# Kernel optimization log

Hardware: AMD Instinct MI355X
Metric: run time of the kernel (lower is better)

The kernel has to match this reference:

```python
import jax, jax.numpy as jnp
import numpy as np

N, E, F, H, D, C = 50000, 800000, 128, 8, 16, 40


def setup_inputs() -> dict:
    key = jax.random.key(0)
    ks = jax.random.split(key, 12)
    s_in = 1.0 / np.sqrt(F)
    s_h = 1.0 / np.sqrt(H * D)
    return {
        "x": jax.random.normal(ks[0], (N, F), jnp.float32),
        "edge_index": jax.random.randint(ks[1], (2, E), 0, N, jnp.int64),
        "W1": jax.random.normal(ks[2], (F, H * D), jnp.float32) * s_in,
        "a_src1": jax.random.normal(ks[3], (H, D), jnp.float32) * s_h,
        "a_dst1": jax.random.normal(ks[4], (H, D), jnp.float32) * s_h,
        "b1": jnp.zeros((H * D,), jnp.float32),
        "W2": jax.random.normal(ks[5], (H * D, H * D), jnp.float32) * s_h,
        "a_src2": jax.random.normal(ks[6], (H, D), jnp.float32) * s_h,
        "a_dst2": jax.random.normal(ks[7], (H, D), jnp.float32) * s_h,
        "b2": jnp.zeros((H * D,), jnp.float32),
        "Wc": jax.random.normal(ks[8], (H * D, C), jnp.float32) * s_h,
        "bc": jnp.zeros((C,), jnp.float32),
    }


def _gat_layer(x, src, dst, W, a_src, a_dst, b):
    # x: [N, F_in]; src/dst: [E'] (self-loops already appended)
    n = x.shape[0]
    h, d = a_src.shape
    hx = (x @ W).reshape(n, h, d)                      # [N, H, D]
    al_src = jnp.einsum("nhd,hd->nh", hx, a_src)       # [N, H]
    al_dst = jnp.einsum("nhd,hd->nh", hx, a_dst)       # [N, H]
    e = jax.nn.leaky_relu(al_src[src] + al_dst[dst], 0.2)  # [E', H]
    # segment softmax over incoming edges of each destination node
    m = jax.ops.segment_max(e, dst, num_segments=n)    # [N, H]
    e = jnp.exp(e - m[dst])
    z = jax.ops.segment_sum(e, dst, num_segments=n)    # [N, H]
    alpha = e / z[dst]                                 # [E', H]
    out = jax.ops.segment_sum(alpha[:, :, None] * hx[src], dst, num_segments=n)
    return out.reshape(n, h * d) + b


def reference(x, edge_index, W1, a_src1, a_dst1, b1, W2, a_src2, a_dst2, b2, Wc, bc):
    n = x.shape[0]
    loops = jnp.arange(n, dtype=edge_index.dtype)
    src = jnp.concatenate([edge_index[0], loops])  # PyG GATConv adds self-loops
    dst = jnp.concatenate([edge_index[1], loops])
    h = _gat_layer(x, src, dst, W1, a_src1, a_dst1, b1)
    h = jax.nn.elu(h)  # ELU between layers (i < K-1); dropout=None -> no-op
    h = _gat_layer(h, src, dst, W2, a_src2, a_dst2, b2)
    return h @ Wc + bc  # [N, C] logits
```

## Files before the change

kernel.cpp:

```cpp
#include <hip/hip_runtime.h>
#include <hip/hip_bf16.h>
#include <hip/hip_fp16.h>


#define FDIM 128
#define HEADS 8

typedef short bf16x8 __attribute__((ext_vector_type(8)));
typedef float f32x4 __attribute__((ext_vector_type(4)));

typedef __attribute__((address_space(1))) const unsigned gu32;
typedef __attribute__((address_space(3))) unsigned lu32;

__device__ __forceinline__ void load_lds16(const void* g, void* l) {
    __builtin_amdgcn_global_load_lds((gu32*)g, (lu32*)l, 16, 0, 0);
}

__device__ __forceinline__ float leaky02(float x) {
    return fmaxf(x, 0.2f * x);
}

__device__ __forceinline__ unsigned pack2h(float x, float y) {
    __half2 h2 = __floats2half2_rn(x, y);
    return *(unsigned*)&h2;
}

__device__ __forceinline__ void split2(float x, unsigned short& hi, unsigned short& lo) {
    unsigned bits = __float_as_uint(x);
    unsigned h = bits + 0x7fffu + ((bits >> 16) & 1u);
    hi = (unsigned short)(h >> 16);
    float hf = __uint_as_float(h & 0xffff0000u);
    float r = x - hf;
    unsigned rb = __float_as_uint(r);
    unsigned l2 = rb + 0x7fffu + ((rb >> 16) & 1u);
    lo = (unsigned short)(l2 >> 16);
}


__global__ __launch_bounds__(256) void wconv_kernel(const float* __restrict__ W1,
                                                    const float* __restrict__ W2,
                                                    unsigned short* __restrict__ w1_hi,
                                                    unsigned short* __restrict__ w1_lo,
                                                    unsigned short* __restrict__ w2_hi,
                                                    unsigned short* __restrict__ w2_lo) {
    int b = blockIdx.x, t = threadIdx.x;
    const float* W = (b < 16) ? W1 : W2;
    unsigned short* whi = (b < 16) ? w1_hi : w2_hi;
    unsigned short* wlo = (b < 16) ? w1_lo : w2_lo;
    int idx = (b & 15) * 256 + t;
    int k = idx >> 5;
    int c0 = (idx & 31) * 4;
#pragma unroll
    for (int i = 0; i < 4; ++i) {
        int c = c0 + i;
        float v = W[k * FDIM + c];
        unsigned short h, l;
        split2(v, h, l);
        int dest = ((k >> 5) * 8 + (c >> 4)) * 512 +
                   ((c & 15) + (((k >> 3) & 3) << 4)) * 8 + (k & 7);
        whi[dest] = h;
        wlo[dest] = l;
    }
}


__global__ __launch_bounds__(256) void scan_partial(const int* __restrict__ deg,
                                                    int* __restrict__ partials,
                                                    int n) {
    __shared__ int red[256];
    int t = threadIdx.x;
    int base = blockIdx.x * 1024 + t * 4;
    int s = 0;
#pragma unroll
    for (int j = 0; j < 4; ++j) {
        int i = base + j;
        if (i < n) s += deg[i];
    }
    red[t] = s;
    __syncthreads();
    for (int off = 128; off > 0; off >>= 1) {
        if (t < off) red[t] += red[t + off];
        __syncthreads();
    }
    if (t == 0) partials[blockIdx.x] = red[0];
}

__global__ __launch_bounds__(256) void scan_final(const int* __restrict__ deg,
                                                  const int* __restrict__ partials,
                                                  int* __restrict__ row_start,
                                                  int n, int nb) {
    __shared__ int sbuf[256];
    __shared__ int boff_s, total_s;
    int t = threadIdx.x;
    if (t < 64) {
        int carry = 0;
        for (int base = 0; base < nb; base += 64) {
            int idx = base + t;
            int v = (idx < nb) ? partials[idx] : 0;
            int incl = v;
#pragma unroll
            for (int off = 1; off < 64; off <<= 1) {
                int x = __shfl_up(incl, off);
                if (t >= off) incl += x;
            }
            if (idx == (int)blockIdx.x) boff_s = carry + incl - v;
            carry += __shfl(incl, 63);
        }
        if (t == 0) total_s = carry;
    }
    __syncthreads();
    if (blockIdx.x == 0 && t == 0) row_start[n] = total_s;

    int base = blockIdx.x * 1024 + t * 4;
    int v[4];
#pragma unroll
    for (int j = 0; j < 4; ++j) v[j] = (base + j < n) ? deg[base + j] : 0;
    int tsum = v[0] + v[1] + v[2] + v[3];
    sbuf[t] = tsum;
    __syncthreads();
    for (int off = 1; off < 256; off <<= 1) {
        int tmp = (t >= off) ? sbuf[t - off] : 0;
        __syncthreads();
        sbuf[t] += tmp;
        __syncthreads();
    }
    int toff = boff_s + sbuf[t] - tsum;
    int run = 0;
#pragma unroll
    for (int j = 0; j < 4; ++j) {
        int i = base + j;
        if (i < n) row_start[i] = toff + run;
        run += v[j];
    }
}


__global__ __launch_bounds__(256) void scatter_kernel(const int* __restrict__ ei,
                                                      const int* __restrict__ rank,
                                                      const int* __restrict__ row_start,
                                                      int* __restrict__ csr_src,
                                                      int E) {
    int tid = threadIdx.x;
#pragma unroll
    for (int j = 0; j < 4; ++j) {
        int e = blockIdx.x * 1024 + j * 256 + tid;
        if (e < E) {
            int s = ei[e];
            int d = ei[E + e];
            __builtin_nontemporal_store(s, &csr_src[row_start[d] + rank[e]]);
        }
    }
}


template <bool FUSED>
__global__ __launch_bounds__(256, 3) void gemm_mfma(const float* __restrict__ xf,
                                                    const unsigned short* __restrict__ a_hi,
                                                    const unsigned short* __restrict__ a_lo,
                                                    const unsigned short* __restrict__ w_hi,
                                                    const unsigned short* __restrict__ w_lo,
                                                    const float* __restrict__ asrc,
                                                    const float* __restrict__ adst,
                                                    float* __restrict__ als,
                                                    float* __restrict__ ald,
                                                    unsigned* __restrict__ hxf,
                                                    int n,
                                                    const int* __restrict__ ei,
                                                    int* __restrict__ deg,
                                                    int* __restrict__ rank,
                                                    int E, int ng, int grid) {
    __shared__ __align__(16) char smem[49152];
    int tid = threadIdx.x;
    int gb;
    if (FUSED) {
        int bid = blockIdx.x;
        int t0 = (int)((long long)bid * ng / grid);
        int t1 = (int)((long long)(bid + 1) * ng / grid);
        if (t1 == t0) {
            int sb = bid - t0;
#pragma unroll
            for (int j = 0; j < 4; ++j) {
                int e = sb * 1024 + j * 256 + tid;
                if (e < E) rank[e] = atomicAdd(&deg[ei[E + e]], 1);
            }
            return;
        }
        gb = t0;
    } else {
        gb = blockIdx.x;
    }

    int lane = tid & 63;
    int wave = tid >> 6;
    int l15 = lane & 15;
    int lg = lane >> 4;
    int row0 = gb * 32;

    {
#pragma unroll
        for (int c = 0; c < 4; ++c) {
            int s = wave * 4 + c;
            int kc = s >> 2, fr = (s >> 1) & 1, p = s & 1;
            int rg = row0 + fr * 16 + l15;
            if (rg > n - 1) rg = n - 1;
            if (FUSED) {
                load_lds16(xf + (size_t)rg * FDIM + kc * 32 + lg * 8 + p * 4,
                           smem + (size_t)s * 1024);
            } else {
                const unsigned short* src = p ? a_lo : a_hi;
                load_lds16(src + (size_t)rg * FDIM + kc * 32 + lg * 8,
                           smem + (size_t)s * 1024);
            }
        }
    }

    auto stage_B = [&](int kc, int buf) {
#pragma unroll
        for (int c = 0; c < 4; ++c) {
            int s = wave * 4 + c;
            int FC = s >> 1, p = s & 1;
            const unsigned short* src = p ? w_lo : w_hi;
            load_lds16(src + (size_t)(kc * 8 + FC) * 512 + lane * 8,
                       smem + 16384 + (size_t)buf * 16384 + (size_t)(FC * 2 + p) * 1024);
        }
    };
    stage_B(0, 0);
    __syncthreads();

    f32x4 acc[2][2];
#pragma unroll
    for (int fr = 0; fr < 2; ++fr)
#pragma unroll
        for (int fc = 0; fc < 2; ++fc)
#pragma unroll
            for (int r = 0; r < 4; ++r) acc[fr][fc][r] = 0.f;

#pragma unroll
    for (int kc = 0; kc < 4; ++kc) {
        const int cur = kc & 1;
        if (kc < 3) stage_B(kc + 1, cur ^ 1);

        bf16x8 Ah[2], Al[2];
#pragma unroll
        for (int fr = 0; fr < 2; ++fr) {
            if (FUSED) {
                const float4 v0 = *(const float4*)(smem + (size_t)(kc * 4 + fr * 2) * 1024 + lane * 16);
                const float4 v1 = *(const float4*)(smem + (size_t)(kc * 4 + fr * 2 + 1) * 1024 + lane * 16);
                float vv[8] = {v0.x, v0.y, v0.z, v0.w, v1.x, v1.y, v1.z, v1.w};
#pragma unroll
                for (int j = 0; j < 8; ++j) {
                    unsigned bits = __float_as_uint(vv[j]);
                    Ah[fr][j] = (short)(bits >> 16);
                    float hf = __uint_as_float(bits & 0xffff0000u);
                    Al[fr][j] = (short)(__float_as_uint(vv[j] - hf) >> 16);
                }
            } else {
                Ah[fr] = *(const bf16x8*)(smem + (size_t)(kc * 4 + fr * 2) * 1024 + lane * 16);
                Al[fr] = *(const bf16x8*)(smem + (size_t)(kc * 4 + fr * 2 + 1) * 1024 + lane * 16);
            }
        }
        bf16x8 Bh[2], Bl[2];
#pragma unroll
        for (int fc = 0; fc < 2; ++fc) {
            int FC = wave * 2 + fc;
            const char* bb = smem + 16384 + (size_t)cur * 16384 + (size_t)(FC * 2) * 1024;
            Bh[fc] = *(const bf16x8*)(bb + lane * 16);
            Bl[fc] = *(const bf16x8*)(bb + 1024 + lane * 16);
        }
#pragma unroll
        for (int fr = 0; fr < 2; ++fr)
#pragma unroll
            for (int fc = 0; fc < 2; ++fc) {
                acc[fr][fc] = __builtin_amdgcn_mfma_f32_16x16x32_bf16(
                    Al[fr], Bh[fc], acc[fr][fc], 0, 0, 0);
                acc[fr][fc] = __builtin_amdgcn_mfma_f32_16x16x32_bf16(
                    Ah[fr], Bl[fc], acc[fr][fc], 0, 0, 0);
                acc[fr][fc] = __builtin_amdgcn_mfma_f32_16x16x32_bf16(
                    Ah[fr], Bh[fc], acc[fr][fc], 0, 0, 0);
            }
        __syncthreads();
    }

    float* dump = (float*)(smem + 16384);
#pragma unroll
    for (int fr = 0; fr < 2; ++fr)
#pragma unroll
        for (int fc = 0; fc < 2; ++fc) {
            int col = wave * 32 + fc * 16 + l15;
#pragma unroll
            for (int reg = 0; reg < 4; ++reg) {
                int row = fr * 16 + lg * 4 + reg;
                dump[row * 132 + col] = acc[fr][fc][reg];
            }
        }
    __syncthreads();

    {
        int row = tid >> 3;
        int hd = tid & 7;
        int row_g = row0 + row;
        const float* src = dump + row * 132 + hd * 16;
        float v[16];
#pragma unroll
        for (int j = 0; j < 4; ++j)
            *(float4*)&v[j * 4] = *(const float4*)(src + j * 4);

        if (row_g < n) {
            uint4 p0, p1;
            p0.x = pack2h(v[0], v[1]);
            p0.y = pack2h(v[2], v[3]);
            p0.z = pack2h(v[4], v[5]);
            p0.w = pack2h(v[6], v[7]);
            p1.x = pack2h(v[8], v[9]);
            p1.y = pack2h(v[10], v[11]);
            p1.z = pack2h(v[12], v[13]);
            p1.w = pack2h(v[14], v[15]);
            unsigned* dst = hxf + (size_t)row_g * 64 + hd * 8;
            *(uint4*)dst = p0;
            *(uint4*)(dst + 4) = p1;

            float s0 = 0.f, s1 = 0.f;
#pragma unroll
            for (int j = 0; j < 16; ++j) {
                s0 += v[j] * asrc[hd * 16 + j];
                s1 += v[j] * adst[hd * 16 + j];
            }
            als[row_g * HEADS + hd] = s0;
            ald[row_g * HEADS + hd] = s1;
        }
    }
}


__global__ __launch_bounds__(256, 8) void gemm_cls(const unsigned* __restrict__ h_f16,
                                                   const float* __restrict__ W,
                                                   const float* __restrict__ bias,
                                                   float* __restrict__ out,
                                                   int n) {
    __shared__ float xs[32][136];
    __shared__ float ws[32][48];
    int tid = threadIdx.x;
    int row0 = blockIdx.x * 128;
    int lane = tid & 63;
    int wave = tid >> 6;
    int lane2 = lane * 2;
    int wc = wave * 10;

    float acc[2][10];
#pragma unroll
    for (int i = 0; i < 2; ++i)
#pragma unroll
        for (int j = 0; j < 10; ++j) acc[i][j] = 0.f;

    for (int kc = 0; kc < 128; kc += 32) {
        if (kc) __syncthreads();
#pragma unroll
        for (int it = 0; it < 4; ++it) {
            int idx = it * 256 + tid;
            int r = idx >> 3, kg = (idx & 7) * 4;
            float4 v = make_float4(0.f, 0.f, 0.f, 0.f);
            if (row0 + r < n) {
                uint2 hh = *(const uint2*)&h_f16[(size_t)(row0 + r) * 64 + (kc + kg) / 2];
                float2 a = __half22float2(*(__half2*)&hh.x);
                float2 b = __half22float2(*(__half2*)&hh.y);
                v.x = a.x; v.y = a.y; v.z = b.x; v.w = b.y;
            }
            int col = r ^ kg;
            xs[kg + 0][col] = v.x;
            xs[kg + 1][col] = v.y;
            xs[kg + 2][col] = v.z;
            xs[kg + 3][col] = v.w;
        }
#pragma unroll
        for (int it = 0; it < 6; ++it) {
            int idx = it * 256 + tid;
            int kk = idx / 48, c = idx - kk * 48;
            ws[kk][c] = (c < 40) ? W[(size_t)(kc + kk) * 40 + c] : 0.f;
        }
        __syncthreads();
#pragma unroll
        for (int k = 0; k < 32; ++k) {
            int s = ((k >> 2) & 7) << 2;
            float2 av2 = *(const float2*)&xs[k][lane2 ^ s];
            float av[2] = {av2.x, av2.y};
#pragma unroll
            for (int j = 0; j < 10; ++j) {
                float w = ws[k][wc + j];
                acc[0][j] += av[0] * w;
                acc[1][j] += av[1] * w;
            }
        }
    }

#pragma unroll
    for (int i = 0; i < 2; ++i) {
        int row = row0 + lane2 + i;
        if (row < n) {
#pragma unroll
            for (int j = 0; j < 10; ++j)
                out[(size_t)row * 40 + wc + j] = acc[i][j] + bias[wc + j];
        }
    }
}


template <bool DOELU, bool WRITELO>
__global__ __launch_bounds__(256) void gat_aggregate(const unsigned* __restrict__ hxf,
                                                     const float* __restrict__ als,
                                                     const float* __restrict__ ald,
                                                     const int* __restrict__ row_start,
                                                     const int* __restrict__ csr_src,
                                                     const float* __restrict__ bias,
                                                     unsigned* __restrict__ h_hi,
                                                     unsigned* __restrict__ h_lo,
                                                     int n) {
    int wid = threadIdx.x >> 6;
    int lane = threadIdx.x & 63;
    int node = blockIdx.x * 4 + wid;
    if (node >= n) return;

    int rs = row_start[node];
    int deg = row_start[node + 1] - rs;

    int h = lane & 7;
    int hc = lane >> 3;
    int lq = lane >> 3;
    float ald_h = ald[node * HEADS + h];

    float acc0 = 0.f, acc1 = 0.f, zown = 0.f;
    int total = deg + 1;

    int ii = lq;
    int srcv = (ii < deg) ? csr_src[rs + ii] : node;
    float w = (ii < total) ? __expf(leaky02(als[srcv * HEADS + h] + ald_h)) : 0.f;

    int i0 = 0;
    for (; i0 + 8 <= total; i0 += 8) {
        zown += w;
        int ii_n = i0 + 8 + lq;
        int srcv_n = (ii_n < deg) ? csr_src[rs + ii_n] : node;
#pragma unroll
        for (int e = 0; e < 8; ++e) {
            int s = __builtin_amdgcn_readlane(srcv, e * 8);
            float we = __shfl(w, e * 8 + hc);
            unsigned v = hxf[(size_t)s * 64 + lane];
            float2 f = __half22float2(*(__half2*)&v);
            acc0 += we * f.x;
            acc1 += we * f.y;
        }
        float w_n = (ii_n < total) ? __expf(leaky02(als[srcv_n * HEADS + h] + ald_h)) : 0.f;
        srcv = srcv_n;
        w = w_n;
    }
    int rem = total - i0;
    if (rem > 0) {
        zown += w;
        for (int e = 0; e < rem; ++e) {
            int s = __builtin_amdgcn_readlane(srcv, e * 8);
            float we = __shfl(w, e * 8 + hc);
            unsigned v = hxf[(size_t)s * 64 + lane];
            float2 f = __half22float2(*(__half2*)&v);
            acc0 += we * f.x;
            acc1 += we * f.y;
        }
    }

    zown += __shfl_xor(zown, 8);
    zown += __shfl_xor(zown, 16);
    zown += __shfl_xor(zown, 32);
    float z = __shfl(zown, hc);

    float2 bv = *(const float2*)&bias[2 * lane];
    float o0 = acc0 / z + bv.x;
    float o1 = acc1 / z + bv.y;
    if (DOELU) {
        o0 = o0 > 0.f ? o0 : (__expf(o0) - 1.f);
        o1 = o1 > 0.f ? o1 : (__expf(o1) - 1.f);
    }
    if (WRITELO) {
        unsigned short hh0, ll0, hh1, ll1;
        split2(o0, hh0, ll0);
        split2(o1, hh1, ll1);
        h_hi[(size_t)node * 64 + lane] = (unsigned)hh0 | ((unsigned)hh1 << 16);
        h_lo[(size_t)node * 64 + lane] = (unsigned)ll0 | ((unsigned)ll1 << 16);
    } else {
        h_hi[(size_t)node * 64 + lane] = pack2h(o0, o1);
    }
}


extern "C" void kernel_launch(void* const* d_in, const int* in_sizes, int n_in,
                              void* d_out, int out_size, void* d_ws, size_t ws_size,
                              hipStream_t stream) {
    const float* x      = (const float*)d_in[0];
    const int*   ei     = (const int*)d_in[1];
    const float* W1     = (const float*)d_in[2];
    const float* a_src1 = (const float*)d_in[3];
    const float* a_dst1 = (const float*)d_in[4];
    const float* b1     = (const float*)d_in[5];
    const float* W2     = (const float*)d_in[6];
    const float* a_src2 = (const float*)d_in[7];
    const float* a_dst2 = (const float*)d_in[8];
    const float* b2     = (const float*)d_in[9];
    const float* Wc     = (const float*)d_in[10];
    const float* bc     = (const float*)d_in[11];
    float* out = (float*)d_out;

    const int N = in_sizes[0] / FDIM;
    const int E = in_sizes[1] / 2;
    const int NB = (N + 1023) / 1024;

    unsigned* hxf = (unsigned*)d_ws;
    unsigned* xh_u = hxf + (size_t)N * 64;
    unsigned* xl_u = xh_u + (size_t)N * 64;
    float* als  = (float*)(xl_u + (size_t)N * 64);
    float* ald  = als + (size_t)N * HEADS;
    unsigned short* w1_hi = (unsigned short*)(ald + (size_t)N * HEADS);
    unsigned short* w1_lo = w1_hi + 16384;
    unsigned short* w2_hi = w1_lo + 16384;
    unsigned short* w2_lo = w2_hi + 16384;
    int* deg       = (int*)(w2_lo + 16384);
    int* row_start = deg + N;
    int* partials  = row_start + ((N + 8) & ~3);
    int* rank      = partials + ((NB + 4) & ~3);
    int* csr_src   = rank + E;

    hipMemsetAsync(deg, 0, (size_t)N * sizeof(int), stream);
    wconv_kernel<<<32, 256, 0, stream>>>(W1, W2, w1_hi, w1_lo, w2_hi, w2_lo);

    const int ng = (N + 31) / 32;
    const int hb = (E + 1023) / 1024;
    const int grid1 = ng + hb;
    const int agg_grid = (N + 3) / 4;
    const int cls_grid = (N + 127) / 128;

    gemm_mfma<true><<<grid1, 256, 0, stream>>>(x, nullptr, nullptr,
                                               w1_hi, w1_lo,
                                               a_src1, a_dst1, als, ald, hxf, N,
                                               ei, deg, rank, E, ng, grid1);
    scan_partial<<<NB, 256, 0, stream>>>(deg, partials, N);
    scan_final<<<NB, 256, 0, stream>>>(deg, partials, row_start, N, NB);
    scatter_kernel<<<hb, 256, 0, stream>>>(ei, rank, row_start, csr_src, E);

    gat_aggregate<true, true><<<agg_grid, 256, 0, stream>>>(
        hxf, als, ald, row_start, csr_src, b1, xh_u, xl_u, N);
    gemm_mfma<false><<<ng, 256, 0, stream>>>(nullptr,
                                             (const unsigned short*)xh_u,
                                             (const unsigned short*)xl_u,
                                             w2_hi, w2_lo,
                                             a_src2, a_dst2, als, ald, hxf, N,
                                             nullptr, nullptr, nullptr, 0, ng, ng);
    gat_aggregate<false, false><<<agg_grid, 256, 0, stream>>>(
        hxf, als, ald, row_start, csr_src, b2, xh_u, xl_u, N);
    gemm_cls<<<cls_grid, 256, 0, stream>>>(xh_u, Wc, bc, out, N);
}
```

Measured before the change: 207.4 us.

## Split layer-1 GEMM to overlap CSR scatter and merge scan kernels

The first-layer projection GEMM is now split into two halves. The degree-counting rider blocks run alongside the first half, and the CSR scatter rider blocks run alongside the second half, which removes the standalone scatter launch. The two-pass scan is merged into one kernel in which each block recomputes its prefix offset by summing every earlier degree entry. That redundant prefix sum costs O(N) reads per block, which grows with block index, in exchange for one fewer launch and no partials buffer.

```diff
diff --git a/kernel.cpp b/kernel.cpp
--- a/kernel.cpp
+++ b/kernel.cpp
@@ -64,54 +64,30 @@
 }
 
 
-__global__ __launch_bounds__(256) void scan_partial(const int* __restrict__ deg,
-                                                    int* __restrict__ partials,
-                                                    int n) {
+__global__ __launch_bounds__(256) void scan_fused(const int* __restrict__ deg,
+                                                  int* __restrict__ row_start,
+                                                  int n, int nb) {
     __shared__ int red[256];
+    __shared__ int sbuf[256];
+    __shared__ int boff_s;
     int t = threadIdx.x;
-    int base = blockIdx.x * 1024 + t * 4;
+    int b = blockIdx.x;
+
+    int limit = b * 1024;
+    if (limit > n) limit = n;
     int s = 0;
-#pragma unroll
-    for (int j = 0; j < 4; ++j) {
-        int i = base + j;
-        if (i < n) s += deg[i];
-    }
+    for (int i = t; i < limit; i += 256) s += deg[i];
     red[t] = s;
     __syncthreads();
     for (int off = 128; off > 0; off >>= 1) {
         if (t < off) red[t] += red[t + off];
         __syncthreads();
     }
-    if (t == 0) partials[blockIdx.x] = red[0];
-}
-
-__global__ __launch_bounds__(256) void scan_final(const int* __restrict__ deg,
-                                                  const int* __restrict__ partials,
-                                                  int* __restrict__ row_start,
-                                                  int n, int nb) {
-    __shared__ int sbuf[256];
-    __shared__ int boff_s, total_s;
-    int t = threadIdx.x;
-    if (t < 64) {
-        int carry = 0;
-        for (int base = 0; base < nb; base += 64) {
-            int idx = base + t;
-            int v = (idx < nb) ? partials[idx] : 0;
-            int incl = v;
-#pragma unroll
-            for (int off = 1; off < 64; off <<= 1) {
-                int x = __shfl_up(incl, off);
-                if (t >= off) incl += x;
-            }
-            if (idx == (int)blockIdx.x) boff_s = carry + incl - v;
-            carry += __shfl(incl, 63);
-        }
-        if (t == 0) total_s = carry;
-    }
+    if (t == 0) boff_s = red[0];
     __syncthreads();
-    if (blockIdx.x == 0 && t == 0) row_start[n] = total_s;
-
-    int base = blockIdx.x * 1024 + t * 4;
+    int boff = boff_s;
+
+    int base = b * 1024 + t * 4;
     int v[4];
 #pragma unroll
     for (int j = 0; j < 4; ++j) v[j] = (base + j < n) ? deg[base + j] : 0;
@@ -124,7 +100,7 @@
         sbuf[t] += tmp;
         __syncthreads();
     }
-    int toff = boff_s + sbuf[t] - tsum;
+    int toff = boff + sbuf[t] - tsum;
     int run = 0;
 #pragma unroll
     for (int j = 0; j < 4; ++j) {
@@ -132,28 +108,11 @@
         if (i < n) row_start[i] = toff + run;
         run += v[j];
     }
-}
-
-
-__global__ __launch_bounds__(256) void scatter_kernel(const int* __restrict__ ei,
-                                                      const int* __restrict__ rank,
-                                                      const int* __restrict__ row_start,
-                                                      int* __restrict__ csr_src,
-                                                      int E) {
-    int tid = threadIdx.x;
-#pragma unroll
-    for (int j = 0; j < 4; ++j) {
-        int e = blockIdx.x * 1024 + j * 256 + tid;
-        if (e < E) {
-            int s = ei[e];
-            int d = ei[E + e];
-            __builtin_nontemporal_store(s, &csr_src[row_start[d] + rank[e]]);
-        }
-    }
-}
-
-
-template <bool FUSED>
+    if (b == nb - 1 && t == 255) row_start[n] = boff + sbuf[255];
+}
+
+
+template <bool FUSED, int RIDER>
 __global__ __launch_bounds__(256, 3) void gemm_mfma(const float* __restrict__ xf,
                                                     const unsigned short* __restrict__ a_hi,
                                                     const unsigned short* __restrict__ a_lo,
@@ -168,26 +127,37 @@
                                                     const int* __restrict__ ei,
                                                     int* __restrict__ deg,
                                                     int* __restrict__ rank,
-                                                    int E, int ng, int grid) {
+                                                    const int* __restrict__ row_start,
+                                                    int* __restrict__ csr_src,
+                                                    int E, int ntiles, int tbase,
+                                                    int grid) {
     __shared__ __align__(16) char smem[49152];
     int tid = threadIdx.x;
     int gb;
-    if (FUSED) {
+    if (RIDER != 0) {
         int bid = blockIdx.x;
-        int t0 = (int)((long long)bid * ng / grid);
-        int t1 = (int)((long long)(bid + 1) * ng / grid);
+        int t0 = (int)((long long)bid * ntiles / grid);
+        int t1 = (int)((long long)(bid + 1) * ntiles / grid);
         if (t1 == t0) {
             int sb = bid - t0;
 #pragma unroll
             for (int j = 0; j < 4; ++j) {
                 int e = sb * 1024 + j * 256 + tid;
-                if (e < E) rank[e] = atomicAdd(&deg[ei[E + e]], 1);
+                if (e < E) {
+                    if (RIDER == 1) {
+                        rank[e] = atomicAdd(&deg[ei[E + e]], 1);
+                    } else {
+                        int s = ei[e];
+                        int d = ei[E + e];
+                        __builtin_nontemporal_store(s, &csr_src[row_start[d] + rank[e]]);
+                    }
+                }
             }
             return;
         }
-        gb = t0;
+        gb = tbase + t0;
     } else {
-        gb = blockIdx.x;
+        gb = tbase + blockIdx.x;
     }
 
     int lane = tid & 63;
@@ -528,28 +498,27 @@
     hipMemsetAsync(deg, 0, (size_t)N * sizeof(int), stream);
     wconv_kernel<<<32, 256, 0, stream>>>(W1, W2, w1_hi, w1_lo, w2_hi, w2_lo);
 
-    const int ng = (N + 31) / 32;
-    const int hb = (E + 1023) / 1024;
-    const int grid1 = ng + hb;
+    const int ng  = (N + 31) / 32;
+    const int ngA = ng / 2;
+    const int ngB = ng - ngA;
+    const int hb  = (E + 1023) / 1024;
     const int agg_grid = (N + 3) / 4;
     const int cls_grid = (N + 127) / 128;
 
-    gemm_mfma<true><<<grid1, 256, 0, stream>>>(x, nullptr, nullptr,
-                                               w1_hi, w1_lo,
-                                               a_src1, a_dst1, als, ald, hxf, N,
-                                               ei, deg, rank, E, ng, grid1);
-    scan_partial<<<NB, 256, 0, stream>>>(deg, partials, N);
-    scan_final<<<NB, 256, 0, stream>>>(deg, partials, row_start, N, NB);
-    scatter_kernel<<<hb, 256, 0, stream>>>(ei, rank, row_start, csr_src, E);
+    gemm_mfma<true, 1><<<ngA + hb, 256, 0, stream>>>(
+        x, nullptr, nullptr, w1_hi, w1_lo, a_src1, a_dst1, als, ald, hxf, N,
+        ei, deg, rank, nullptr, nullptr, E, ngA, 0, ngA + hb);
+    scan_fused<<<NB, 256, 0, stream>>>(deg, row_start, N, NB);
+    gemm_mfma<true, 2><<<ngB + hb, 256, 0, stream>>>(
+        x, nullptr, nullptr, w1_hi, w1_lo, a_src1, a_dst1, als, ald, hxf, N,
+        ei, nullptr, rank, row_start, csr_src, E, ngB, ngA, ngB + hb);
 
     gat_aggregate<true, true><<<agg_grid, 256, 0, stream>>>(
         hxf, als, ald, row_start, csr_src, b1, xh_u, xl_u, N);
-    gemm_mfma<false><<<ng, 256, 0, stream>>>(nullptr,
-                                             (const unsigned short*)xh_u,
-                                             (const unsigned short*)xl_u,
-                                             w2_hi, w2_lo,
-                                             a_src2, a_dst2, als, ald, hxf, N,
-                                             nullptr, nullptr, nullptr, 0, ng, ng);
+    gemm_mfma<false, 0><<<ng, 256, 0, stream>>>(
+        nullptr, (const unsigned short*)xh_u, (const unsigned short*)xl_u,
+        w2_hi, w2_lo, a_src2, a_dst2, als, ald, hxf, N,
+        nullptr, nullptr, nullptr, nullptr, nullptr, 0, ng, 0, ng);
     gat_aggregate<false, false><<<agg_grid, 256, 0, stream>>>(
         hxf, als, ald, row_start, csr_src, b2, xh_u, xl_u, N);
     gemm_cls<<<cls_grid, 256, 0, stream>>>(xh_u, Wc, bc, out, N);
```

Measured after the change: 233.6 us. 12.6% more time.
